# Kernel tuning notes

Hardware: AMD Instinct MI355X
Metric: run time of the kernel (lower is better)

Reference implementation:

```python
import jax, jax.numpy as jnp
import numpy as np

ALPHA = 0.1
THETA = 0.5
N_NODES = 50000
N_EDGES = 320000
IN_F, HID, OUT_F, N_LAYERS = 50, 256, 121, 4


def setup_inputs() -> dict:
    key = jax.random.key(0)
    ks = jax.random.split(key, 8)
    x = jax.random.normal(ks[0], (N_NODES, IN_F), dtype=jnp.float32)
    edge_index = jax.random.randint(ks[1], (2, N_EDGES), 0, N_NODES, dtype=jnp.int64)
    edge_weight = jax.random.uniform(ks[2], (N_EDGES,), dtype=jnp.float32) / 8.0  # ~normalized adj values
    lin0_w = jax.random.normal(ks[3], (IN_F, HID), dtype=jnp.float32) / np.sqrt(IN_F)
    lin0_b = jnp.zeros((HID,), dtype=jnp.float32)
    W = jax.random.normal(ks[4], (N_LAYERS, HID, HID), dtype=jnp.float32) / np.sqrt(HID)
    lin1_w = jax.random.normal(ks[5], (HID, OUT_F), dtype=jnp.float32) / np.sqrt(HID)
    lin1_b = jnp.zeros((OUT_F,), dtype=jnp.float32)
    return {"x": x, "edge_index": edge_index, "edge_weight": edge_weight,
            "lin0_w": lin0_w, "lin0_b": lin0_b, "W": W,
            "lin1_w": lin1_w, "lin1_b": lin1_b}


def reference(x, edge_index, edge_weight, lin0_w, lin0_b, W, lin1_w, lin1_b):
    # Eval mode: dropout is identity.
    n = x.shape[0]
    src, dst = edge_index[0], edge_index[1]
    x0 = jax.nn.relu(x @ lin0_w + lin0_b)          # [N, H] initial residual
    h = x0
    for l in range(W.shape[0]):
        beta = jnp.log(THETA / (l + 1) + 1.0)       # GCN2Conv beta, layer = l+1
        # sparse adj propagation: agg[i] = sum_{e: dst=i} w_e * h[src_e]
        agg = jax.ops.segment_sum(edge_weight[:, None] * h[src], dst, num_segments=n)
        s = (1.0 - ALPHA) * agg + ALPHA * x0        # initial-residual mixing
        out = (1.0 - beta) * s + beta * (s @ W[l])  # identity-mapped weight (shared)
        h = jax.nn.relu(out + h)                    # outer residual + relu
    return h @ lin1_w + lin1_b                      # [N, num_classes]
```

## Files before the change

kernel.cpp:

```cpp
#include <hip/hip_runtime.h>
#include <math.h>

#define IN_F   50
#define HID    256
#define OUT_F  121
#define N_LAYERS 4
#define K0PAD  64

typedef __attribute__((ext_vector_type(8))) short short8;
typedef __attribute__((ext_vector_type(8))) ushort ushort8;
typedef __attribute__((ext_vector_type(4))) float f32x4;

#define GLOBAL_AS __attribute__((address_space(1)))
#define LDS_AS    __attribute__((address_space(3)))

__device__ __forceinline__ ushort f2bf(float f) {
    union { float f; unsigned u; } c; c.f = f;
    unsigned u = c.u;
    u += 0x7fffu + ((u >> 16) & 1u);
    return (ushort)(u >> 16);
}
__device__ __forceinline__ float bf2f(ushort u) {
    union { unsigned u; float f; } c; c.u = ((unsigned)u) << 16;
    return c.f;
}

__global__ void hist_kernel(const int* __restrict__ dst, int* __restrict__ counts, int E) {
    int e = blockIdx.x * blockDim.x + threadIdx.x;
    if (e < E) atomicAdd(&counts[dst[e]], 1);
}

__global__ void scan_phase1(const int* __restrict__ counts, int* __restrict__ row_ptr,
                            int* __restrict__ bsum, int n) {
    __shared__ int sd[1024];
    int t = threadIdx.x;
    int i = blockIdx.x * 1024 + t;
    int v = (i < n) ? counts[i] : 0;
    sd[t] = v;
    __syncthreads();
    for (int off = 1; off < 1024; off <<= 1) {
        int tmp = (t >= off) ? sd[t - off] : 0;
        __syncthreads();
        sd[t] += tmp;
        __syncthreads();
    }
    if (i < n) row_ptr[i] = sd[t] - v;
    if (t == 1023) bsum[blockIdx.x] = sd[1023];
}

__global__ void scan_phase2(int* __restrict__ bsum, int nb) {
    __shared__ int sd[64];
    int t = threadIdx.x;
    int v = (t < nb) ? bsum[t] : 0;
    sd[t] = v;
    __syncthreads();
    for (int off = 1; off < 64; off <<= 1) {
        int tmp = (t >= off) ? sd[t - off] : 0;
        __syncthreads();
        sd[t] += tmp;
        __syncthreads();
    }
    if (t < nb) bsum[t] = sd[t] - v;
    if (t == nb - 1) bsum[nb] = sd[t];
}

__global__ void scan_phase3(int* __restrict__ row_ptr, int* __restrict__ cursor,
                            const int* __restrict__ bsum, int n, int nb) {
    int i = blockIdx.x * 1024 + threadIdx.x;
    if (i < n) {
        int v = row_ptr[i] + bsum[blockIdx.x];
        row_ptr[i] = v;
        cursor[i]  = v;
    }
    if (i == n - 1) row_ptr[n] = bsum[nb];
}

__global__ void scatter_kernel(const int* __restrict__ src, const int* __restrict__ dst,
                               const float* __restrict__ ew, int* __restrict__ cursor,
                               int* __restrict__ col, float* __restrict__ wv, int E) {
    int e = blockIdx.x * blockDim.x + threadIdx.x;
    if (e < E) {
        int d = dst[e];
        int pos = atomicAdd(&cursor[d], 1);
        col[pos] = src[e];
        wv[pos] = ew[e];
    }
}

__global__ void convert_x_kernel(const float* __restrict__ x, ushort* __restrict__ x_bf, int n) {
    int i = blockIdx.x * 256 + threadIdx.x;
    int nd = i >> 6, k = i & 63;
    if (nd < n) x_bf[i] = (k < IN_F) ? f2bf(x[(size_t)nd * IN_F + k]) : 0;
}

__global__ void convert_w0_kernel(const float* __restrict__ w, ushort* __restrict__ wt0) {
    int nn = blockIdx.x;
    int k = threadIdx.x;
    float v = (k < IN_F) ? w[(size_t)k * HID + nn] : 0.f;
    wt0[(size_t)nn * K0PAD + k] = f2bf(v);
}

__global__ void convert_w_kernel(const float* __restrict__ W, ushort* __restrict__ Wt) {
    int nn = blockIdx.x, l = blockIdx.y, k = threadIdx.x;
    float beta = logf(0.5f / (float)(l + 1) + 1.0f);
    float v = beta * W[(size_t)l * HID * HID + (size_t)k * HID + nn];
    if (k == nn) v += 1.0f - beta;
    Wt[(size_t)l * HID * HID + (size_t)nn * HID + k] = f2bf(v);
}

__global__ void convert_w1_kernel(const float* __restrict__ w1, ushort* __restrict__ Wt1) {
    int nn = blockIdx.x;
    int k = threadIdx.x;
    float v = (nn < OUT_F) ? w1[(size_t)k * OUT_F + nn] : 0.f;
    Wt1[(size_t)nn * HID + k] = f2bf(v);
}

__global__ __launch_bounds__(256) void lin0_mfma(
        const ushort* __restrict__ x_bf, const ushort* __restrict__ wt0,
        const float* __restrict__ b, ushort* __restrict__ x0_bf,
        ushort* __restrict__ h_bf, int M) {
    __shared__ ushort As[4][128][8];
    __shared__ ushort Bs[4][128][8];
    int tid = threadIdx.x;
    int wave = tid >> 6;
    int lane = tid & 63;
    int r16 = lane & 15, q = lane >> 4;
    int bm = blockIdx.x * 128;
    int bn = blockIdx.y * 128;
    int wm = (wave >> 1) * 64, wn = (wave & 1) * 64;

    f32x4 acc[4][4] = {};

    int srow = tid & 127;
    int koff0 = tid >> 7;
    int arow = bm + srow; if (arow >= M) arow = M - 1;
    const ushort* aptr = x_bf + (size_t)arow * K0PAD;
    const ushort* bptr = wt0 + (size_t)(bn + srow) * K0PAD;
    char* AsB = (char*)&As[0][0][0];
    char* BsB = (char*)&Bs[0][0][0];
    int woff = wave * 1024;

    const short8* As8 = (const short8*)&As[0][0][0];
    const short8* Bs8 = (const short8*)&Bs[0][0][0];

    for (int k0 = 0; k0 < K0PAD; k0 += 32) {
        __builtin_amdgcn_global_load_lds((const GLOBAL_AS void*)(aptr + k0 + koff0 * 8),
                                         (LDS_AS void*)(AsB + woff), 16, 0, 0);
        __builtin_amdgcn_global_load_lds((const GLOBAL_AS void*)(aptr + k0 + (koff0 + 2) * 8),
                                         (LDS_AS void*)(AsB + 4096 + woff), 16, 0, 0);
        __builtin_amdgcn_global_load_lds((const GLOBAL_AS void*)(bptr + k0 + koff0 * 8),
                                         (LDS_AS void*)(BsB + woff), 16, 0, 0);
        __builtin_amdgcn_global_load_lds((const GLOBAL_AS void*)(bptr + k0 + (koff0 + 2) * 8),
                                         (LDS_AS void*)(BsB + 4096 + woff), 16, 0, 0);
        __syncthreads();

        short8 av[4], bv[4];
#pragma unroll
        for (int mf = 0; mf < 4; ++mf)
            av[mf] = As8[q * 128 + wm + mf * 16 + r16];
#pragma unroll
        for (int nf = 0; nf < 4; ++nf)
            bv[nf] = Bs8[q * 128 + wn + nf * 16 + r16];
#pragma unroll
        for (int mf = 0; mf < 4; ++mf)
#pragma unroll
            for (int nf = 0; nf < 4; ++nf)
                acc[mf][nf] = __builtin_amdgcn_mfma_f32_16x16x32_bf16(av[mf], bv[nf], acc[mf][nf], 0, 0, 0);
        __syncthreads();
    }

#pragma unroll
    for (int mf = 0; mf < 4; ++mf) {
#pragma unroll
        for (int j = 0; j < 4; ++j) {
            int row = bm + wm + mf * 16 + q * 4 + j;
            if (row >= M) continue;
#pragma unroll
            for (int nf = 0; nf < 4; ++nf) {
                int c = bn + wn + nf * 16 + r16;
                size_t idx = (size_t)row * HID + c;
                ushort v = f2bf(fmaxf(acc[mf][nf][j] + b[c], 0.f));
                x0_bf[idx] = v;
                h_bf[idx]  = v;
            }
        }
    }
}

__global__ __launch_bounds__(256) void spmm_mix_kernel(
        const int* __restrict__ row_ptr, const int* __restrict__ col,
        const float* __restrict__ wv, const ushort* __restrict__ h_bf,
        const ushort* __restrict__ x0_bf, ushort* __restrict__ s_bf, int n) {
    int node = (blockIdx.x * 256 + threadIdx.x) >> 6;
    if (node >= n) return;
    int lane = threadIdx.x & 63;
    int half = lane >> 5;
    int l32 = lane & 31;
    int f0 = l32 * 8;
    int beg = row_ptr[node], end = row_ptr[node + 1];

    float a[8] = {};

#define PAIR(B)                                                                   \
    {                                                                             \
        int my_e = (B) + half;                                                    \
        int ce = my_e < end ? my_e : end - 1;                                     \
        float w = (my_e < end) ? wv[ce] : 0.f;                                    \
        int c = col[ce];                                                          \
        ushort8 v = *reinterpret_cast<const ushort8*>(&h_bf[(size_t)c * HID + f0]); \
        _Pragma("unroll")                                                         \
        for (int i = 0; i < 8; ++i) a[i] = fmaf(w, bf2f(v[i]), a[i]);             \
    }

    int base = beg;
    for (; base + 4 <= end; base += 4) {
        PAIR(base);
        PAIR(base + 2);
    }
    if (base < end) { PAIR(base); base += 2; }
    if (base < end) { PAIR(base); }
#undef PAIR

#pragma unroll
    for (int i = 0; i < 8; ++i)
        a[i] += __shfl_xor(a[i], 32, 64);

    if (half == 0) {
        size_t idx = (size_t)node * HID + f0;
        ushort8 xv = *reinterpret_cast<const ushort8*>(&x0_bf[idx]);
        ushort8 r;
#pragma unroll
        for (int i = 0; i < 8; ++i)
            r[i] = f2bf(0.9f * a[i] + 0.1f * bf2f(xv[i]));
        *reinterpret_cast<ushort8*>(&s_bf[idx]) = r;
    }
}

__global__ __launch_bounds__(256) void gemm_mfma_layer(
        const ushort* __restrict__ s_bf, const ushort* __restrict__ wt,
        ushort* __restrict__ h_bf, int M) {
    __shared__ ushort As[4][128][8];
    __shared__ ushort Bs[4][128][8];
    int tid = threadIdx.x;
    int wave = tid >> 6;
    int lane = tid & 63;
    int r16 = lane & 15, q = lane >> 4;
    int bm = blockIdx.x * 128;
    int bn = blockIdx.y * 128;
    int wm = (wave >> 1) * 64, wn = (wave & 1) * 64;

    f32x4 acc[4][4] = {};

    int srow = tid & 127;
    int koff0 = tid >> 7;
    int arow = bm + srow; if (arow >= M) arow = M - 1;
    const ushort* aptr = s_bf + (size_t)arow * HID;
    const ushort* bptr = wt + (size_t)(bn + srow) * HID;
    char* AsB = (char*)&As[0][0][0];
    char* BsB = (char*)&Bs[0][0][0];
    int woff = wave * 1024;

    const short8* As8 = (const short8*)&As[0][0][0];
    const short8* Bs8 = (const short8*)&Bs[0][0][0];

    for (int k0 = 0; k0 < HID; k0 += 32) {
        __builtin_amdgcn_global_load_lds((const GLOBAL_AS void*)(aptr + k0 + koff0 * 8),
                                         (LDS_AS void*)(AsB + woff), 16, 0, 0);
        __builtin_amdgcn_global_load_lds((const GLOBAL_AS void*)(aptr + k0 + (koff0 + 2) * 8),
                                         (LDS_AS void*)(AsB + 4096 + woff), 16, 0, 0);
        __builtin_amdgcn_global_load_lds((const GLOBAL_AS void*)(bptr + k0 + koff0 * 8),
                                         (LDS_AS void*)(BsB + woff), 16, 0, 0);
        __builtin_amdgcn_global_load_lds((const GLOBAL_AS void*)(bptr + k0 + (koff0 + 2) * 8),
                                         (LDS_AS void*)(BsB + 4096 + woff), 16, 0, 0);
        __syncthreads();

        short8 av[4], bv[4];
#pragma unroll
        for (int mf = 0; mf < 4; ++mf)
            av[mf] = As8[q * 128 + wm + mf * 16 + r16];
#pragma unroll
        for (int nf = 0; nf < 4; ++nf)
            bv[nf] = Bs8[q * 128 + wn + nf * 16 + r16];
#pragma unroll
        for (int mf = 0; mf < 4; ++mf)
#pragma unroll
            for (int nf = 0; nf < 4; ++nf)
                acc[mf][nf] = __builtin_amdgcn_mfma_f32_16x16x32_bf16(av[mf], bv[nf], acc[mf][nf], 0, 0, 0);
        __syncthreads();
    }

#pragma unroll
    for (int mf = 0; mf < 4; ++mf) {
#pragma unroll
        for (int j = 0; j < 4; ++j) {
            int row = bm + wm + mf * 16 + q * 4 + j;
            if (row >= M) continue;
#pragma unroll
            for (int nf = 0; nf < 4; ++nf) {
                int c = bn + wn + nf * 16 + r16;
                size_t idx = (size_t)row * HID + c;
                float v = fmaxf(acc[mf][nf][j] + bf2f(h_bf[idx]), 0.f);
                h_bf[idx] = f2bf(v);
            }
        }
    }
}

__global__ __launch_bounds__(256) void lin1_mfma(
        const ushort* __restrict__ h_bf, const ushort* __restrict__ wt1,
        const float* __restrict__ b, float* __restrict__ out, int M) {
    __shared__ ushort As[4][128][8];
    __shared__ ushort Bs[4][128][8];
    int tid = threadIdx.x;
    int wave = tid >> 6;
    int lane = tid & 63;
    int r16 = lane & 15, q = lane >> 4;
    int bm = blockIdx.x * 128;
    int wm = (wave >> 1) * 64, wn = (wave & 1) * 64;

    f32x4 acc[4][4] = {};

    int srow = tid & 127;
    int koff0 = tid >> 7;
    int arow = bm + srow; if (arow >= M) arow = M - 1;
    const ushort* aptr = h_bf + (size_t)arow * HID;
    const ushort* bptr = wt1 + (size_t)srow * HID;
    char* AsB = (char*)&As[0][0][0];
    char* BsB = (char*)&Bs[0][0][0];
    int woff = wave * 1024;

    const short8* As8 = (const short8*)&As[0][0][0];
    const short8* Bs8 = (const short8*)&Bs[0][0][0];

    for (int k0 = 0; k0 < HID; k0 += 32) {
        __builtin_amdgcn_global_load_lds((const GLOBAL_AS void*)(aptr + k0 + koff0 * 8),
                                         (LDS_AS void*)(AsB + woff), 16, 0, 0);
        __builtin_amdgcn_global_load_lds((const GLOBAL_AS void*)(aptr + k0 + (koff0 + 2) * 8),
                                         (LDS_AS void*)(AsB + 4096 + woff), 16, 0, 0);
        __builtin_amdgcn_global_load_lds((const GLOBAL_AS void*)(bptr + k0 + koff0 * 8),
                                         (LDS_AS void*)(BsB + woff), 16, 0, 0);
        __builtin_amdgcn_global_load_lds((const GLOBAL_AS void*)(bptr + k0 + (koff0 + 2) * 8),
                                         (LDS_AS void*)(BsB + 4096 + woff), 16, 0, 0);
        __syncthreads();

        short8 av[4], bv[4];
#pragma unroll
        for (int mf = 0; mf < 4; ++mf)
            av[mf] = As8[q * 128 + wm + mf * 16 + r16];
#pragma unroll
        for (int nf = 0; nf < 4; ++nf)
            bv[nf] = Bs8[q * 128 + wn + nf * 16 + r16];
#pragma unroll
        for (int mf = 0; mf < 4; ++mf)
#pragma unroll
            for (int nf = 0; nf < 4; ++nf)
                acc[mf][nf] = __builtin_amdgcn_mfma_f32_16x16x32_bf16(av[mf], bv[nf], acc[mf][nf], 0, 0, 0);
        __syncthreads();
    }

#pragma unroll
    for (int mf = 0; mf < 4; ++mf) {
#pragma unroll
        for (int j = 0; j < 4; ++j) {
            int row = bm + wm + mf * 16 + q * 4 + j;
            if (row >= M) continue;
#pragma unroll
            for (int nf = 0; nf < 4; ++nf) {
                int c = wn + nf * 16 + r16;
                if (c < OUT_F)
                    out[(size_t)row * OUT_F + c] = acc[mf][nf][j] + b[c];
            }
        }
    }
}

extern "C" void kernel_launch(void* const* d_in, const int* in_sizes, int n_in,
                              void* d_out, int out_size, void* d_ws, size_t ws_size,
                              hipStream_t stream) {
    const float* x      = (const float*)d_in[0];
    const int*   ei     = (const int*)d_in[1];
    const float* ew     = (const float*)d_in[2];
    const float* lin0_w = (const float*)d_in[3];
    const float* lin0_b = (const float*)d_in[4];
    const float* W      = (const float*)d_in[5];
    const float* lin1_w = (const float*)d_in[6];
    const float* lin1_b = (const float*)d_in[7];
    float* out = (float*)d_out;

    int N = in_sizes[0] / IN_F;
    int E = in_sizes[2];
    const int* src = ei;
    const int* dst = ei + E;

    char* ws = (char*)d_ws;
    ushort* x0_bf   = (ushort*)ws; ws += (size_t)N * HID * 2;
    ushort* h_bf    = (ushort*)ws; ws += (size_t)N * HID * 2;
    ushort* s_bf    = (ushort*)ws; ws += (size_t)N * HID * 2;
    ushort* x_bf    = (ushort*)ws; ws += (size_t)N * K0PAD * 2;
    ushort* Wt0     = (ushort*)ws; ws += (size_t)HID * K0PAD * 2;
    ushort* Wt      = (ushort*)ws; ws += (size_t)N_LAYERS * HID * HID * 2;
    ushort* Wt1     = (ushort*)ws; ws += (size_t)128 * HID * 2;
    int*    row_ptr = (int*)ws;    ws += (size_t)(N + 1) * 4;
    int*    counts  = (int*)ws;    ws += (size_t)N * 4;
    int*    cursor  = (int*)ws;    ws += (size_t)N * 4;
    int*    bsum    = (int*)ws;    ws += (size_t)128 * 4;
    int*    col     = (int*)ws;    ws += (size_t)E * 4;
    float*  wv      = (float*)ws;  ws += (size_t)E * 4;

    int nb = (N + 1023) / 1024;

    hipMemsetAsync(counts, 0, (size_t)N * 4, stream);
    hist_kernel<<<(E + 255) / 256, 256, 0, stream>>>(dst, counts, E);
    scan_phase1<<<nb, 1024, 0, stream>>>(counts, row_ptr, bsum, N);
    scan_phase2<<<1, 64, 0, stream>>>(bsum, nb);
    scan_phase3<<<nb, 1024, 0, stream>>>(row_ptr, cursor, bsum, N, nb);
    scatter_kernel<<<(E + 255) / 256, 256, 0, stream>>>(src, dst, ew, cursor, col, wv, E);

    convert_x_kernel<<<(N * K0PAD + 255) / 256, 256, 0, stream>>>(x, x_bf, N);
    convert_w0_kernel<<<HID, K0PAD, 0, stream>>>(lin0_w, Wt0);
    convert_w_kernel<<<dim3(HID, N_LAYERS), HID, 0, stream>>>(W, Wt);
    convert_w1_kernel<<<128, HID, 0, stream>>>(lin1_w, Wt1);

    int mblocks = (N + 127) / 128;
    lin0_mfma<<<dim3(mblocks, 2), 256, 0, stream>>>(x_bf, Wt0, lin0_b, x0_bf, h_bf, N);

    for (int l = 0; l < N_LAYERS; ++l) {
        spmm_mix_kernel<<<(N + 3) / 4, 256, 0, stream>>>(row_ptr, col, wv, h_bf, x0_bf, s_bf, N);
        gemm_mfma_layer<<<dim3(mblocks, 2), 256, 0, stream>>>(
            s_bf, Wt + (size_t)l * HID * HID, h_bf, N);
    }

    lin1_mfma<<<mblocks, 256, 0, stream>>>(h_bf, Wt1, lin1_b, out, N);
}
```

Baseline: 357.5 us.

## Split SpMM into feature slices per block and fuse prep conversion kernels

The SpMM is restructured so each block handles a 32-feature slice (one of eight) for 32 nodes. Each wave walks 8 nodes, with four sub-groups of 16 lanes splitting the edges and each lane loading two bf16 features. Slicing by feature shrinks the gathered working set per block, which should improve L2 locality of the h gathers, but the 4-byte gathers are narrower than the old 16-byte loads and every edge index and weight is now read eight times. Separately, the four weight/input conversion kernels and the counts memset are merged into a single flat prep kernel to cut launch overhead.

```diff
diff --git a/kernel.cpp b/kernel.cpp
--- a/kernel.cpp
+++ b/kernel.cpp
@@ -8,7 +8,6 @@
 #define K0PAD  64
 
 typedef __attribute__((ext_vector_type(8))) short short8;
-typedef __attribute__((ext_vector_type(8))) ushort ushort8;
 typedef __attribute__((ext_vector_type(4))) float f32x4;
 
 #define GLOBAL_AS __attribute__((address_space(1)))
@@ -23,6 +22,46 @@
 __device__ __forceinline__ float bf2f(ushort u) {
     union { unsigned u; float f; } c; c.u = ((unsigned)u) << 16;
     return c.f;
+}
+
+__global__ __launch_bounds__(256) void prep_kernel(
+        const float* __restrict__ x, const float* __restrict__ w0,
+        const float* __restrict__ W, const float* __restrict__ w1,
+        ushort* __restrict__ x_bf, ushort* __restrict__ wt0,
+        ushort* __restrict__ Wt, ushort* __restrict__ wt1,
+        int* __restrict__ counts, int n) {
+    long long flat = (long long)blockIdx.x * 256 + threadIdx.x;
+    long long r0 = (long long)n * K0PAD;
+    if (flat < r0) {
+        int nd = (int)(flat >> 6), k = (int)(flat & 63);
+        x_bf[flat] = (k < IN_F) ? f2bf(x[(size_t)nd * IN_F + k]) : 0;
+        return;
+    }
+    flat -= r0;
+    if (flat < HID * K0PAD) {
+        int nn = (int)(flat >> 6), k = (int)(flat & 63);
+        wt0[flat] = (k < IN_F) ? f2bf(w0[(size_t)k * HID + nn]) : 0;
+        return;
+    }
+    flat -= HID * K0PAD;
+    if (flat < N_LAYERS * HID * HID) {
+        int l = (int)(flat >> 16);
+        int rem = (int)(flat & 65535);
+        int nn = rem >> 8, k = rem & 255;
+        float beta = logf(0.5f / (float)(l + 1) + 1.0f);
+        float v = beta * W[(size_t)l * HID * HID + (size_t)k * HID + nn];
+        if (k == nn) v += 1.0f - beta;
+        Wt[flat] = f2bf(v);
+        return;
+    }
+    flat -= N_LAYERS * HID * HID;
+    if (flat < 128 * HID) {
+        int nn = (int)(flat >> 8), k = (int)(flat & 255);
+        wt1[flat] = (nn < OUT_F) ? f2bf(w1[(size_t)k * OUT_F + nn]) : 0;
+        return;
+    }
+    flat -= 128 * HID;
+    if (flat < n) counts[flat] = 0;
 }
 
 __global__ void hist_kernel(const int* __restrict__ dst, int* __restrict__ counts, int E) {
@@ -85,34 +124,6 @@
         col[pos] = src[e];
         wv[pos] = ew[e];
     }
-}
-
-__global__ void convert_x_kernel(const float* __restrict__ x, ushort* __restrict__ x_bf, int n) {
-    int i = blockIdx.x * 256 + threadIdx.x;
-    int nd = i >> 6, k = i & 63;
-    if (nd < n) x_bf[i] = (k < IN_F) ? f2bf(x[(size_t)nd * IN_F + k]) : 0;
-}
-
-__global__ void convert_w0_kernel(const float* __restrict__ w, ushort* __restrict__ wt0) {
-    int nn = blockIdx.x;
-    int k = threadIdx.x;
-    float v = (k < IN_F) ? w[(size_t)k * HID + nn] : 0.f;
-    wt0[(size_t)nn * K0PAD + k] = f2bf(v);
-}
-
-__global__ void convert_w_kernel(const float* __restrict__ W, ushort* __restrict__ Wt) {
-    int nn = blockIdx.x, l = blockIdx.y, k = threadIdx.x;
-    float beta = logf(0.5f / (float)(l + 1) + 1.0f);
-    float v = beta * W[(size_t)l * HID * HID + (size_t)k * HID + nn];
-    if (k == nn) v += 1.0f - beta;
-    Wt[(size_t)l * HID * HID + (size_t)nn * HID + k] = f2bf(v);
-}
-
-__global__ void convert_w1_kernel(const float* __restrict__ w1, ushort* __restrict__ Wt1) {
-    int nn = blockIdx.x;
-    int k = threadIdx.x;
-    float v = (nn < OUT_F) ? w1[(size_t)k * OUT_F + nn] : 0.f;
-    Wt1[(size_t)nn * HID + k] = f2bf(v);
 }
 
 __global__ __launch_bounds__(256) void lin0_mfma(
@@ -191,48 +202,38 @@
         const int* __restrict__ row_ptr, const int* __restrict__ col,
         const float* __restrict__ wv, const ushort* __restrict__ h_bf,
         const ushort* __restrict__ x0_bf, ushort* __restrict__ s_bf, int n) {
-    int node = (blockIdx.x * 256 + threadIdx.x) >> 6;
-    if (node >= n) return;
-    int lane = threadIdx.x & 63;
-    int half = lane >> 5;
-    int l32 = lane & 31;
-    int f0 = l32 * 8;
-    int beg = row_ptr[node], end = row_ptr[node + 1];
-
-    float a[8] = {};
-
-#define PAIR(B)                                                                   \
-    {                                                                             \
-        int my_e = (B) + half;                                                    \
-        int ce = my_e < end ? my_e : end - 1;                                     \
-        float w = (my_e < end) ? wv[ce] : 0.f;                                    \
-        int c = col[ce];                                                          \
-        ushort8 v = *reinterpret_cast<const ushort8*>(&h_bf[(size_t)c * HID + f0]); \
-        _Pragma("unroll")                                                         \
-        for (int i = 0; i < 8; ++i) a[i] = fmaf(w, bf2f(v[i]), a[i]);             \
-    }
-
-    int base = beg;
-    for (; base + 4 <= end; base += 4) {
-        PAIR(base);
-        PAIR(base + 2);
-    }
-    if (base < end) { PAIR(base); base += 2; }
-    if (base < end) { PAIR(base); }
-#undef PAIR
-
-#pragma unroll
-    for (int i = 0; i < 8; ++i)
-        a[i] += __shfl_xor(a[i], 32, 64);
-
-    if (half == 0) {
-        size_t idx = (size_t)node * HID + f0;
-        ushort8 xv = *reinterpret_cast<const ushort8*>(&x0_bf[idx]);
-        ushort8 r;
-#pragma unroll
-        for (int i = 0; i < 8; ++i)
-            r[i] = f2bf(0.9f * a[i] + 0.1f * bf2f(xv[i]));
-        *reinterpret_cast<ushort8*>(&s_bf[idx]) = r;
+    int slice = blockIdx.x & 7;
+    int ng    = blockIdx.x >> 3;
+    int wave  = threadIdx.x >> 6;
+    int lane  = threadIdx.x & 63;
+    int sub   = lane >> 4;
+    int fl    = lane & 15;
+    int fcol  = slice * 32 + fl * 2;
+    int node0 = (ng * 4 + wave) * 8;
+    for (int i = 0; i < 8; ++i) {
+        int node = node0 + i;
+        if (node >= n) return;
+        int beg = row_ptr[node], end = row_ptr[node + 1];
+        float a0 = 0.f, a1 = 0.f;
+        for (int e = beg; e < end; e += 4) {
+            int ee = e + sub;
+            int ce = (ee < end) ? ee : e;
+            float w = (ee < end) ? wv[ee] : 0.f;
+            int c = col[ce];
+            ushort2 v = *reinterpret_cast<const ushort2*>(&h_bf[(size_t)c * HID + fcol]);
+            a0 = fmaf(w, bf2f(v.x), a0);
+            a1 = fmaf(w, bf2f(v.y), a1);
+        }
+        a0 += __shfl_xor(a0, 16, 64); a0 += __shfl_xor(a0, 32, 64);
+        a1 += __shfl_xor(a1, 16, 64); a1 += __shfl_xor(a1, 32, 64);
+        if (sub == 0) {
+            size_t idx = (size_t)node * HID + fcol;
+            ushort2 xv = *reinterpret_cast<const ushort2*>(&x0_bf[idx]);
+            ushort2 r;
+            r.x = f2bf(0.9f * a0 + 0.1f * bf2f(xv.x));
+            r.y = f2bf(0.9f * a1 + 0.1f * bf2f(xv.y));
+            *reinterpret_cast<ushort2*>(&s_bf[idx]) = r;
+        }
     }
 }
 
@@ -409,23 +410,23 @@
 
     int nb = (N + 1023) / 1024;
 
-    hipMemsetAsync(counts, 0, (size_t)N * 4, stream);
+    size_t prep_tot = (size_t)N * K0PAD + HID * K0PAD
+                    + (size_t)N_LAYERS * HID * HID + 128 * HID + N;
+    prep_kernel<<<(int)((prep_tot + 255) / 256), 256, 0, stream>>>(
+        x, lin0_w, W, lin1_w, x_bf, Wt0, Wt, Wt1, counts, N);
+
     hist_kernel<<<(E + 255) / 256, 256, 0, stream>>>(dst, counts, E);
     scan_phase1<<<nb, 1024, 0, stream>>>(counts, row_ptr, bsum, N);
     scan_phase2<<<1, 64, 0, stream>>>(bsum, nb);
     scan_phase3<<<nb, 1024, 0, stream>>>(row_ptr, cursor, bsum, N, nb);
     scatter_kernel<<<(E + 255) / 256, 256, 0, stream>>>(src, dst, ew, cursor, col, wv, E);
 
-    convert_x_kernel<<<(N * K0PAD + 255) / 256, 256, 0, stream>>>(x, x_bf, N);
-    convert_w0_kernel<<<HID, K0PAD, 0, stream>>>(lin0_w, Wt0);
-    convert_w_kernel<<<dim3(HID, N_LAYERS), HID, 0, stream>>>(W, Wt);
-    convert_w1_kernel<<<128, HID, 0, stream>>>(lin1_w, Wt1);
-
     int mblocks = (N + 127) / 128;
     lin0_mfma<<<dim3(mblocks, 2), 256, 0, stream>>>(x_bf, Wt0, lin0_b, x0_bf, h_bf, N);
 
+    int spmm_blocks = 8 * ((N + 31) / 32);
     for (int l = 0; l < N_LAYERS; ++l) {
-        spmm_mix_kernel<<<(N + 3) / 4, 256, 0, stream>>>(row_ptr, col, wv, h_bf, x0_bf, s_bf, N);
+        spmm_mix_kernel<<<spmm_blocks, 256, 0, stream>>>(row_ptr, col, wv, h_bf, x0_bf, s_bf, N);
         gemm_mfma_layer<<<dim3(mblocks, 2), 256, 0, stream>>>(
             s_bf, Wt + (size_t)l * HID * HID, h_bf, N);
     }
```

After: 687.5 us. 92.3% more time.
